# Kernel optimization log

Measured on AMD Instinct MI355X. Metric: run time of the kernel, lower is better.

Reference implementation:

```python
import jax, jax.numpy as jnp
import numpy as np

VOCAB, E, H, HOPS, HEADS = 32000, 128, 256, 3, 4
N, TM, WLEN, TQ = 32, 50, 20, 20


def _gru(x_tbe, h0, Wih, Whh, bih, bhh):
    # x_tbe: [T, B, E] time-major; h0: [B, H]. PyTorch GRU gate order (r, z, n).
    def step(h, xt):
        gi = xt @ Wih.T + bih
        gh = h @ Whh.T + bhh
        ir, iz, inn = jnp.split(gi, 3, axis=-1)
        hr, hz, hn = jnp.split(gh, 3, axis=-1)
        r = jax.nn.sigmoid(ir + hr)
        z = jax.nn.sigmoid(iz + hz)
        n = jnp.tanh(inn + r * hn)
        return (1.0 - z) * n + z * h, None
    h, _ = jax.lax.scan(step, h0, x_tbe)
    return h


def setup_inputs() -> dict:
    key = jax.random.key(0)
    ks = jax.random.split(key, 24)
    f32 = jnp.float32
    emb = jax.random.uniform(ks[0], (VOCAB, E), f32, -3 ** 0.5, 3 ** 0.5)
    emb = emb.at[0].set(0.0)  # padding_idx=0
    s = 0.05
    inp = {
        'stories': jax.random.randint(ks[1], (N, TM, WLEN), 0, VOCAB),
        'questions': jax.random.randint(ks[2], (N, TQ), 0, VOCAB),
        'emb': emb,
        'q_Wih': jax.random.normal(ks[3], (3 * H, E), f32) * s,
        'q_Whh': jax.random.normal(ks[4], (3 * H, H), f32) * s,
        'q_bih': jnp.zeros((3 * H,), f32),
        'q_bhh': jnp.zeros((3 * H,), f32),
        'i_Wih': jax.random.normal(ks[5], (3 * H, E), f32) * s,
        'i_Whh': jax.random.normal(ks[6], (3 * H, H), f32) * s,
        'i_bih': jnp.zeros((3 * H,), f32),
        'i_bhh': jnp.zeros((3 * H,), f32),
        'Wm': jax.random.normal(ks[7], (HOPS, HEADS, H, H), f32) * s,
        'Wo_w': jax.random.normal(ks[8], (HOPS, H, HEADS * H), f32) * s,
        'Wo_b': jnp.full((HOPS, H), 0.01, f32),
        'ft_W1': jax.random.normal(ks[9], (H, H), f32) * s,
        'ft_b1': jnp.full((H,), 0.01, f32),
        'ft_W2': jax.random.normal(ks[10], (H, H), f32) * s,
        'ft_b2': jnp.full((H,), 0.01, f32),
        'g_W1': jax.random.normal(ks[11], (3 * H, 3 * H), f32) * s,
        'g_b1': jnp.full((3 * H,), 0.01, f32),
        'g_W2': jax.random.normal(ks[12], (3 * H, 3 * H), f32) * s,
        'g_b2': jnp.full((3 * H,), 0.01, f32),
        'V_w': jax.random.normal(ks[13], (VOCAB, 3 * H), f32) * s,
    }
    return inp


def reference(stories, questions, emb, q_Wih, q_Whh, q_bih, q_bhh,
              i_Wih, i_Whh, i_bih, i_bhh, Wm, Wo_w, Wo_b,
              ft_W1, ft_b1, ft_W2, ft_b2, g_W1, g_b1, g_W2, g_b2, V_w):
    n, tm, _ = stories.shape
    h = i_Whh.shape[1]
    hops, heads = Wm.shape[0], Wm.shape[1]

    # ---- input module: per-batch-item GRU; hidden state carries across batch items (as in source loop) ----
    story_embs = emb[stories]  # [N, TM, W, E]
    def bstep(hid, se):  # se: [TM, W, E]
        hid2 = _gru(jnp.swapaxes(se, 0, 1), hid, i_Wih, i_Whh, i_bih, i_bhh)
        return hid2, hid2
    _, memory = jax.lax.scan(bstep, jnp.zeros((tm, h), emb.dtype), story_embs)  # [N, TM, H]

    # ---- question module ----
    q_emb = emb[questions]  # [N, TQ, E]
    q = _gru(jnp.swapaxes(q_emb, 0, 1), jnp.zeros((n, h), emb.dtype), q_Wih, q_Whh, q_bih, q_bhh)  # [N, H]

    def ft(x):
        return jax.nn.relu(jax.nn.relu(x @ ft_W1.T + ft_b1) @ ft_W2.T + ft_b2)

    # ---- multi-hop attention controllers ----
    o_k = ft(q)
    buffers = []
    for hp in range(hops):
        proj = jnp.tanh(jnp.einsum('ntd,hed->nhte', memory, Wm[hp]))      # [N,heads,TM,H]
        scores = jax.nn.softmax(jnp.einsum('nhte,ne->nht', proj, o_k), axis=-1)
        rep = jnp.einsum('nht,ntd->nhd', scores, memory)                   # [N,heads,H]
        buf = rep.reshape(n, heads * h) @ Wo_w[hp].T + Wo_b[hp]            # [N,H]
        buffers.append(buf)
        o_k = ft(buf)
    wb = jnp.stack(buffers, axis=1)  # [N, HOPS, H]

    # ---- RM: all-pairs relation MLP (dropout = identity in eval) ----
    npair = hops * hops
    left = jnp.broadcast_to(wb[:, None, :, :], (n, hops, hops, h)).reshape(n, npair, h)
    right = jnp.broadcast_to(wb[:, :, None, :], (n, hops, hops, h)).reshape(n, npair, h)
    qx = jnp.broadcast_to(q[:, None, :], (n, npair, h))
    comb = jnp.concatenate([left, right, qx], axis=-1)                     # [N, HOPS^2, 3H]
    g = jax.nn.relu(jax.nn.relu(comb @ g_W1.T + g_b1) @ g_W2.T + g_b2)
    reasoning = g.sum(axis=1)                                              # [N, 3H]
    return reasoning @ V_w.T                                               # [N, VOCAB]
```

## Files before the change

### kernel.cpp

```cpp
#include <hip/hip_runtime.h>
#include <cmath>

#define VOCABN 32000
#define EE 128
#define HH 256
#define H3 768
#define HOPSN 3
#define HEADSN 4
#define NB 32
#define TMN 50
#define WLENN 20
#define TQN 20
#define NPOS (NB*TMN*WLENN)
#define NQPOS (NB*TQN)

#define OFF_MEM    0
#define OFF_Q      (OFF_MEM + NB*TMN*HH)
#define OFF_OK     (OFF_Q + NB*HH)
#define OFF_WB     (OFF_OK + NB*HH)
#define OFF_REP    (OFF_WB + NB*HOPSN*HH)
#define OFF_REAS   (OFF_REP + NB*HEADSN*HH)
#define OFF_Y1     (OFF_REAS + NB*H3)
#define OFF_PROJ   (OFF_Y1 + NB*9*H3)
#define OFF_GI     (OFF_PROJ + NB*12*TMN*HH)

typedef __fp16 h2 __attribute__((ext_vector_type(2)));

__device__ __forceinline__ float sigm(float x) { return 1.f / (1.f + expf(-x)); }

__device__ __forceinline__ unsigned packh2(float x, float y) {
    h2 h = __builtin_amdgcn_cvt_pkrtz(x, y);
    return __builtin_bit_cast(unsigned, h);
}

__device__ __forceinline__ float fdot2u(unsigned a, unsigned b, float c) {
    return __builtin_amdgcn_fdot2(__builtin_bit_cast(h2, a),
                                  __builtin_bit_cast(h2, b), c, false);
}

#define LW(v, base, i8) { const float4 A_ = reinterpret_cast<const float4*>(base)[2*(i8)];     \
                          const float4 B_ = reinterpret_cast<const float4*>(base)[2*(i8)+1];   \
                          v.x = packh2(A_.x, A_.y); v.y = packh2(A_.z, A_.w);                  \
                          v.z = packh2(B_.x, B_.y); v.w = packh2(B_.z, B_.w); }

#define GIB 64
__global__ __launch_bounds__(768) void k_gi(const int* __restrict__ stories,
                                            const int* __restrict__ questions,
                                            const float* __restrict__ emb,
                                            const float* __restrict__ iWih,
                                            const float* __restrict__ qWih,
                                            const float* __restrict__ ibih, const float* __restrict__ ibhh,
                                            const float* __restrict__ qbih, const float* __restrict__ qbhh,
                                            float* __restrict__ ws)
{
    __shared__ unsigned xs[GIB][EE / 2];
    __fp16* __restrict__ gi = (__fp16*)(ws + OFF_GI);
    const int j = threadIdx.x;
    const bool isq = blockIdx.x >= (NPOS / GIB);
    const int pblk = isq ? (blockIdx.x - NPOS / GIB) : blockIdx.x;
    const int p0 = pblk * GIB;
    const size_t g0 = (isq ? (size_t)NPOS : 0) + (size_t)p0;
    const int* __restrict__ toks = isq ? (questions + p0) : (stories + p0);
    const float* __restrict__ Wih = isq ? qWih : iWih;
    const float* __restrict__ bih = isq ? qbih : ibih;
    const float* __restrict__ bhh = isq ? qbhh : ibhh;
    const float bias = (j < 2 * HH) ? (bih[j] + bhh[j]) : bih[j];
    const float* wrowp = Wih + (size_t)j * EE;
    uint4 v_0, v_1, v_2, v_3, v_4, v_5, v_6, v_7, v_8, v_9, v_10, v_11, v_12, v_13, v_14, v_15;
    LW(v_0, wrowp, 0)  LW(v_1, wrowp, 1)  LW(v_2, wrowp, 2)  LW(v_3, wrowp, 3)
    LW(v_4, wrowp, 4)  LW(v_5, wrowp, 5)  LW(v_6, wrowp, 6)  LW(v_7, wrowp, 7)
    LW(v_8, wrowp, 8)  LW(v_9, wrowp, 9)  LW(v_10, wrowp, 10) LW(v_11, wrowp, 11)
    LW(v_12, wrowp, 12) LW(v_13, wrowp, 13) LW(v_14, wrowp, 14) LW(v_15, wrowp, 15)

    for (int idx = j; idx < GIB * (EE / 2); idx += H3) {
        const int p = idx >> 6, c = idx & 63;
        const int tok = toks[p];
        const float2 e2 = reinterpret_cast<const float2*>(emb + (size_t)tok * EE)[c];
        xs[p][c] = packh2(e2.x, e2.y);
    }
    __syncthreads();

#define DOTG(i) { const uint4 xv = x4[i];                                     \
    acc = fdot2u(xv.x, v_##i.x, acc); acc = fdot2u(xv.y, v_##i.y, acc);       \
    acc = fdot2u(xv.z, v_##i.z, acc); acc = fdot2u(xv.w, v_##i.w, acc); }

    for (int p = 0; p < GIB; ++p) {
        const uint4* x4 = reinterpret_cast<const uint4*>(&xs[p][0]);
        float acc = bias;
        DOTG(0)  DOTG(1)  DOTG(2)  DOTG(3)  DOTG(4)  DOTG(5)  DOTG(6)  DOTG(7)
        DOTG(8)  DOTG(9)  DOTG(10) DOTG(11) DOTG(12) DOTG(13) DOTG(14) DOTG(15)
        gi[(g0 + p) * H3 + j] = (__fp16)acc;
    }
#undef DOTG
}

#define LDSF 22016
__global__ __attribute__((amdgpu_flat_work_group_size(512, 512), amdgpu_waves_per_eu(1, 1)))
void k_gru9(
    const float* __restrict__ iWhh, const float* __restrict__ qWhh,
    const float* __restrict__ ibhh, const float* __restrict__ qbhh,
    float* __restrict__ ws)
{
    __shared__ float ldsb[LDSF];
    unsigned* hp32 = (unsigned*)ldsb;
    float* red = ldsb + 128;
    const int tid = threadIdx.x;
    const int j = tid & 255, kh = tid >> 8;
    const int blk = blockIdx.x;
    const bool isq = blk >= TMN;
    const float* __restrict__ Whh = isq ? qWhh : iWhh;
    const float* row0 = Whh + (size_t)j * HH + kh * 128;
    const float* row1 = Whh + (size_t)(HH + j) * HH + kh * 128;
    const float* row2 = Whh + (size_t)(2 * HH + j) * HH + kh * 128;
    uint4 w0_0, w0_1, w0_2, w0_3, w0_4, w0_5, w0_6, w0_7,
          w0_8, w0_9, w0_10, w0_11, w0_12, w0_13, w0_14, w0_15;
    uint4 w1_0, w1_1, w1_2, w1_3, w1_4, w1_5, w1_6, w1_7,
          w1_8, w1_9, w1_10, w1_11, w1_12, w1_13, w1_14, w1_15;
    uint4 w2_0, w2_1, w2_2, w2_3, w2_4, w2_5, w2_6, w2_7,
          w2_8, w2_9, w2_10, w2_11, w2_12, w2_13, w2_14, w2_15;
    LW(w0_0, row0, 0)  LW(w0_1, row0, 1)  LW(w0_2, row0, 2)  LW(w0_3, row0, 3)
    LW(w0_4, row0, 4)  LW(w0_5, row0, 5)  LW(w0_6, row0, 6)  LW(w0_7, row0, 7)
    LW(w0_8, row0, 8)  LW(w0_9, row0, 9)  LW(w0_10, row0, 10) LW(w0_11, row0, 11)
    LW(w0_12, row0, 12) LW(w0_13, row0, 13) LW(w0_14, row0, 14) LW(w0_15, row0, 15)
    LW(w1_0, row1, 0)  LW(w1_1, row1, 1)  LW(w1_2, row1, 2)  LW(w1_3, row1, 3)
    LW(w1_4, row1, 4)  LW(w1_5, row1, 5)  LW(w1_6, row1, 6)  LW(w1_7, row1, 7)
    LW(w1_8, row1, 8)  LW(w1_9, row1, 9)  LW(w1_10, row1, 10) LW(w1_11, row1, 11)
    LW(w1_12, row1, 12) LW(w1_13, row1, 13) LW(w1_14, row1, 14) LW(w1_15, row1, 15)
    LW(w2_0, row2, 0)  LW(w2_1, row2, 1)  LW(w2_2, row2, 2)  LW(w2_3, row2, 3)
    LW(w2_4, row2, 4)  LW(w2_5, row2, 5)  LW(w2_6, row2, 6)  LW(w2_7, row2, 7)
    LW(w2_8, row2, 8)  LW(w2_9, row2, 9)  LW(w2_10, row2, 10) LW(w2_11, row2, 11)
    LW(w2_12, row2, 12) LW(w2_13, row2, 13) LW(w2_14, row2, 14) LW(w2_15, row2, 15)

    float bnH = 0.f, hstate = 0.f;
    if (kh == 0) bnH = (isq ? qbhh : ibhh)[2 * HH + j];
    if (tid < HH / 2) hp32[tid] = 0u;
    const __fp16* __restrict__ gib = (const __fp16*)(ws + OFF_GI)
                                     + (isq ? (size_t)NPOS * H3 : 0);
    float* __restrict__ memv = ws + OFF_MEM;
    float* __restrict__ qv   = ws + OFF_Q;
    __syncthreads();

#define DOT(i) { const uint4 hv = hp4[kh * 16 + (i)];                        \
    a0 = fdot2u(hv.x, w0_##i.x, a0); a0 = fdot2u(hv.y, w0_##i.y, a0);        \
    a0 = fdot2u(hv.z, w0_##i.z, a0); a0 = fdot2u(hv.w, w0_##i.w, a0);        \
    a1 = fdot2u(hv.x, w1_##i.x, a1); a1 = fdot2u(hv.y, w1_##i.y, a1);        \
    a1 = fdot2u(hv.z, w1_##i.z, a1); a1 = fdot2u(hv.w, w1_##i.w, a1);        \
    a2 = fdot2u(hv.x, w2_##i.x, a2); a2 = fdot2u(hv.y, w2_##i.y, a2);        \
    a2 = fdot2u(hv.z, w2_##i.z, a2); a2 = fdot2u(hv.w, w2_##i.w, a2); }

    const int nOuter = isq ? 1 : NB;
    const int c = isq ? (blk - TMN) : blk;
    for (int n = 0; n < nOuter; ++n) {
        for (int t = 0; t < WLENN; ++t) {
            const int pos = isq ? (c * TQN + t) : ((n * TMN + c) * WLENN + t);
            float gir = 0.f, giz = 0.f, gin = 0.f;
            if (kh == 0) {
                const size_t gb = (size_t)pos * H3;
                gir = (float)gib[gb + j];
                giz = (float)gib[gb + HH + j];
                gin = (float)gib[gb + 2 * HH + j];
            }
            float a0 = 0.f, a1 = 0.f, a2 = 0.f;
            const uint4* hp4 = reinterpret_cast<const uint4*>(hp32);
            DOT(0)  DOT(1)  DOT(2)  DOT(3)  DOT(4)  DOT(5)  DOT(6)  DOT(7)
            DOT(8)  DOT(9)  DOT(10) DOT(11) DOT(12) DOT(13) DOT(14) DOT(15)
            if (kh == 1) { red[j * 5 + 0] = a0; red[j * 5 + 1] = a1; red[j * 5 + 2] = a2; }
            __syncthreads();
            if (kh == 0) {
                const float* rr = red + j * 5;
                const float r  = sigm(a0 + rr[0] + gir);
                const float z  = sigm(a1 + rr[1] + giz);
                const float nn = tanhf(gin + r * (a2 + rr[2] + bnH));
                hstate = (1.f - z) * nn + z * hstate;
                reinterpret_cast<__fp16*>(hp32)[j] = (__fp16)hstate;
                if (t == WLENN - 1) {
                    if (isq) qv[c * HH + j] = hstate;
                    else     memv[(size_t)(n * TMN + c) * HH + j] = hstate;
                }
            }
            __syncthreads();
        }
    }
#undef DOT
}

__global__ __launch_bounds__(256) void k_ft(const float* __restrict__ src, float* __restrict__ dst,
                                            const float* __restrict__ W1, const float* __restrict__ b1,
                                            const float* __restrict__ W2, const float* __restrict__ b2)
{
    __shared__ float xr[HH];
    __shared__ float y1[HH];
    const int n = blockIdx.x, j = threadIdx.x;
    xr[j] = src[n * HH + j];
    __syncthreads();
    float acc = b1[j];
    const float4* w1 = reinterpret_cast<const float4*>(W1 + j * HH);
    #pragma unroll 4
    for (int k4 = 0; k4 < HH / 4; ++k4) {
        const float4 w = w1[k4];
        const float4 x = *reinterpret_cast<const float4*>(&xr[k4 * 4]);
        acc = fmaf(x.x, w.x, fmaf(x.y, w.y, fmaf(x.z, w.z, fmaf(x.w, w.w, acc))));
    }
    y1[j] = fmaxf(acc, 0.f);
    __syncthreads();
    acc = b2[j];
    const float4* w2 = reinterpret_cast<const float4*>(W2 + j * HH);
    #pragma unroll 4
    for (int k4 = 0; k4 < HH / 4; ++k4) {
        const float4 w = w2[k4];
        const float4 x = *reinterpret_cast<const float4*>(&y1[k4 * 4]);
        acc = fmaf(x.x, w.x, fmaf(x.y, w.y, fmaf(x.z, w.z, fmaf(x.w, w.w, acc))));
    }
    dst[n * HH + j] = fmaxf(acc, 0.f);
}

__global__ __launch_bounds__(256) void k_proj(const float* __restrict__ Wm, float* __restrict__ ws)
{
    __shared__ float mem_s[TMN][HH];
    const int n = blockIdx.x / 12, he = blockIdx.x % 12;
    const int e = threadIdx.x;
    const float* __restrict__ memory = ws + OFF_MEM + n * TMN * HH;
    for (int idx = e; idx < TMN * HH; idx += HH)
        (&mem_s[0][0])[idx] = memory[idx];
    __syncthreads();
    float p[TMN];
    #pragma unroll
    for (int t = 0; t < TMN; ++t) p[t] = 0.f;
    const float4* wrow = reinterpret_cast<const float4*>(Wm + ((size_t)he * HH + e) * HH);
    for (int d4 = 0; d4 < HH / 4; ++d4) {
        const float4 w = wrow[d4];
        #pragma unroll
        for (int t = 0; t < TMN; ++t) {
            const float4 m = *reinterpret_cast<const float4*>(&mem_s[t][d4 * 4]);
            p[t] = fmaf(m.x, w.x, fmaf(m.y, w.y, fmaf(m.z, w.z, fmaf(m.w, w.w, p[t]))));
        }
    }
    float* __restrict__ proj = ws + OFF_PROJ + ((size_t)(n * 12 + he) * TMN) * HH;
    #pragma unroll
    for (int t = 0; t < TMN; ++t) proj[t * HH + e] = tanhf(p[t]);
}

__global__ __launch_bounds__(256) void k_attn2(float* __restrict__ ws, int hp)
{
    __shared__ float wred[4][TMN];
    __shared__ float sc[TMN];
    const int n = blockIdx.x / HEADSN, hh = blockIdx.x % HEADSN;
    const int e = threadIdx.x;
    const float* __restrict__ proj = ws + OFF_PROJ + ((size_t)(n * 12 + hp * HEADSN + hh) * TMN) * HH;
    const float* __restrict__ memory = ws + OFF_MEM + n * TMN * HH;
    const float okv = (ws + OFF_OK)[n * HH + e];
    const int lane = e & 63, wv = e >> 6;
    #pragma unroll 10
    for (int t = 0; t < TMN; ++t) {
        float v = proj[t * HH + e] * okv;
        #pragma unroll
        for (int off = 32; off > 0; off >>= 1) v += __shfl_xor(v, off);
        if (lane == 0) wred[wv][t] = v;
    }
    __syncthreads();
    if (e < TMN) sc[e] = wred[0][e] + wred[1][e] + wred[2][e] + wred[3][e];
    __syncthreads();
    if (e == 0) {
        float mx = sc[0];
        for (int t = 1; t < TMN; ++t) mx = fmaxf(mx, sc[t]);
        float sum = 0.f;
        for (int t = 0; t < TMN; ++t) { const float ex = expf(sc[t] - mx); sc[t] = ex; sum += ex; }
        const float inv = 1.f / sum;
        for (int t = 0; t < TMN; ++t) sc[t] *= inv;
    }
    __syncthreads();
    float r = 0.f;
    #pragma unroll 10
    for (int t = 0; t < TMN; ++t) r = fmaf(sc[t], memory[t * HH + e], r);
    (ws + OFF_REP)[(n * HEADSN + hh) * HH + e] = r;
}

__global__ __launch_bounds__(256) void k_buf(const float* __restrict__ Wo_w, const float* __restrict__ Wo_b,
                                             const float* __restrict__ W1, const float* __restrict__ b1,
                                             const float* __restrict__ W2, const float* __restrict__ b2,
                                             float* __restrict__ ws, int hp)
{
    __shared__ float repf[HEADSN * HH];
    __shared__ float bufs[HH];
    __shared__ float y1[HH];
    const int n = blockIdx.x, j = threadIdx.x;
    const float* __restrict__ rep = ws + OFF_REP + n * HEADSN * HH;
    for (int idx = j; idx < HEADSN * HH; idx += HH) repf[idx] = rep[idx];
    __syncthreads();
    float acc = Wo_b[hp * HH + j];
    const float4* wrow = reinterpret_cast<const float4*>(Wo_w + ((size_t)hp * HH + j) * (HEADSN * HH));
    #pragma unroll 4
    for (int c4 = 0; c4 < HEADSN * HH / 4; ++c4) {
        const float4 w = wrow[c4];
        const float4 x = *reinterpret_cast<const float4*>(&repf[c4 * 4]);
        acc = fmaf(x.x, w.x, fmaf(x.y, w.y, fmaf(x.z, w.z, fmaf(x.w, w.w, acc))));
    }
    (ws + OFF_WB)[(n * HOPSN + hp) * HH + j] = acc;
    bufs[j] = acc;
    __syncthreads();
    float a1 = b1[j];
    const float4* w1 = reinterpret_cast<const float4*>(W1 + j * HH);
    #pragma unroll 4
    for (int k4 = 0; k4 < HH / 4; ++k4) {
        const float4 w = w1[k4];
        const float4 x = *reinterpret_cast<const float4*>(&bufs[k4 * 4]);
        a1 = fmaf(x.x, w.x, fmaf(x.y, w.y, fmaf(x.z, w.z, fmaf(x.w, w.w, a1))));
    }
    y1[j] = fmaxf(a1, 0.f);
    __syncthreads();
    float a2 = b2[j];
    const float4* w2 = reinterpret_cast<const float4*>(W2 + j * HH);
    #pragma unroll 4
    for (int k4 = 0; k4 < HH / 4; ++k4) {
        const float4 w = w2[k4];
        const float4 x = *reinterpret_cast<const float4*>(&y1[k4 * 4]);
        a2 = fmaf(x.x, w.x, fmaf(x.y, w.y, fmaf(x.z, w.z, fmaf(x.w, w.w, a2))));
    }
    (ws + OFF_OK)[n * HH + j] = fmaxf(a2, 0.f);
}

__global__ __launch_bounds__(256) void k_rm1(const float* __restrict__ gW1, const float* __restrict__ gb1,
                                             float* __restrict__ ws)
{
    __shared__ float comb[9 * H3];
    const int n = blockIdx.x / 3, ot = blockIdx.x % 3;
    const int o = ot * 256 + threadIdx.x;
    const float* __restrict__ wb = ws + OFF_WB + n * HOPSN * HH;
    const float* __restrict__ qv = ws + OFF_Q + n * HH;
    for (int idx = threadIdx.x; idx < 9 * H3; idx += 256) {
        const int p = idx / H3, cc = idx - p * H3;
        const int ii = p / 3, jj = p % 3;
        float v;
        if (cc < HH)           v = wb[jj * HH + cc];
        else if (cc < 2 * HH)  v = wb[ii * HH + (cc - HH)];
        else                   v = qv[cc - 2 * HH];
        comb[idx] = v;
    }
    __syncthreads();
    float acc[9];
    const float b = gb1[o];
    #pragma unroll
    for (int p = 0; p < 9; ++p) acc[p] = b;
    const float4* w1 = reinterpret_cast<const float4*>(gW1 + (size_t)o * H3);
    for (int c4 = 0; c4 < H3 / 4; ++c4) {
        const float4 w = w1[c4];
        #pragma unroll
        for (int p = 0; p < 9; ++p) {
            const float4 x = *reinterpret_cast<const float4*>(&comb[p * H3 + c4 * 4]);
            acc[p] = fmaf(x.x, w.x, fmaf(x.y, w.y, fmaf(x.z, w.z, fmaf(x.w, w.w, acc[p]))));
        }
    }
    float* __restrict__ y1 = ws + OFF_Y1 + (size_t)n * 9 * H3;
    #pragma unroll
    for (int p = 0; p < 9; ++p) y1[p * H3 + o] = fmaxf(acc[p], 0.f);
}

__global__ __launch_bounds__(256) void k_rm2(const float* __restrict__ gW2, const float* __restrict__ gb2,
                                             float* __restrict__ ws)
{
    __shared__ float y1s[9 * H3];
    const int n = blockIdx.x / 3, ot = blockIdx.x % 3;
    const int o = ot * 256 + threadIdx.x;
    const float* __restrict__ y1 = ws + OFF_Y1 + (size_t)n * 9 * H3;
    for (int idx = threadIdx.x; idx < 9 * H3; idx += 256) y1s[idx] = y1[idx];
    __syncthreads();
    float acc[9];
    const float b = gb2[o];
    #pragma unroll
    for (int p = 0; p < 9; ++p) acc[p] = b;
    const float4* w2 = reinterpret_cast<const float4*>(gW2 + (size_t)o * H3);
    for (int c4 = 0; c4 < H3 / 4; ++c4) {
        const float4 w = w2[c4];
        #pragma unroll
        for (int p = 0; p < 9; ++p) {
            const float4 x = *reinterpret_cast<const float4*>(&y1s[p * H3 + c4 * 4]);
            acc[p] = fmaf(x.x, w.x, fmaf(x.y, w.y, fmaf(x.z, w.z, fmaf(x.w, w.w, acc[p]))));
        }
    }
    float s = 0.f;
    #pragma unroll
    for (int p = 0; p < 9; ++p) s += fmaxf(acc[p], 0.f);
    (ws + OFF_REAS)[n * H3 + o] = s;
}

#define RST 36
__global__ __launch_bounds__(256) void k_out(const float* __restrict__ V_w, const float* __restrict__ ws,
                                             float* __restrict__ out)
{
    __shared__ float rsT[H3 * RST];
    const int tid = threadIdx.x;
    const int v = blockIdx.x * 128 + (tid & 127);
    const int nh = tid >> 7;
    for (int idx = tid; idx < NB * H3; idx += 256) {
        const int n = idx / H3, d = idx - n * H3;
        rsT[d * RST + n] = (ws + OFF_REAS)[idx];
    }
    __syncthreads();
    float acc[16];
    #pragma unroll
    for (int i = 0; i < 16; ++i) acc[i] = 0.f;
    const float4* vw = reinterpret_cast<const float4*>(V_w + (size_t)v * H3);
    for (int d4 = 0; d4 < H3 / 4; ++d4) {
        const float4 w = vw[d4];
        #pragma unroll
        for (int dd = 0; dd < 4; ++dd) {
            const float wd = (dd == 0) ? w.x : (dd == 1) ? w.y : (dd == 2) ? w.z : w.w;
            const float* rr = &rsT[(d4 * 4 + dd) * RST + nh * 16];
            #pragma unroll
            for (int q = 0; q < 4; ++q) {
                const float4 r4 = *reinterpret_cast<const float4*>(rr + 4 * q);
                acc[4 * q + 0] = fmaf(wd, r4.x, acc[4 * q + 0]);
                acc[4 * q + 1] = fmaf(wd, r4.y, acc[4 * q + 1]);
                acc[4 * q + 2] = fmaf(wd, r4.z, acc[4 * q + 2]);
                acc[4 * q + 3] = fmaf(wd, r4.w, acc[4 * q + 3]);
            }
        }
    }
    #pragma unroll
    for (int i = 0; i < 16; ++i)
        out[(size_t)(nh * 16 + i) * VOCABN + v] = acc[i];
}

extern "C" void kernel_launch(void* const* d_in, const int* in_sizes, int n_in,
                              void* d_out, int out_size, void* d_ws, size_t ws_size,
                              hipStream_t stream)
{
    const int*   stories   = (const int*)d_in[0];
    const int*   questions = (const int*)d_in[1];
    const float* emb   = (const float*)d_in[2];
    const float* qWih  = (const float*)d_in[3];
    const float* qWhh  = (const float*)d_in[4];
    const float* qbih  = (const float*)d_in[5];
    const float* qbhh  = (const float*)d_in[6];
    const float* iWih  = (const float*)d_in[7];
    const float* iWhh  = (const float*)d_in[8];
    const float* ibih  = (const float*)d_in[9];
    const float* ibhh  = (const float*)d_in[10];
    const float* Wm    = (const float*)d_in[11];
    const float* Wo_w  = (const float*)d_in[12];
    const float* Wo_b  = (const float*)d_in[13];
    const float* ftW1  = (const float*)d_in[14];
    const float* ftb1  = (const float*)d_in[15];
    const float* ftW2  = (const float*)d_in[16];
    const float* ftb2  = (const float*)d_in[17];
    const float* gW1   = (const float*)d_in[18];
    const float* gb1   = (const float*)d_in[19];
    const float* gW2   = (const float*)d_in[20];
    const float* gb2   = (const float*)d_in[21];
    const float* V_w   = (const float*)d_in[22];
    float* ws  = (float*)d_ws;
    float* out = (float*)d_out;

    hipLaunchKernelGGL(k_gi, dim3((NPOS + NQPOS) / GIB), dim3(H3), 0, stream,
                       stories, questions, emb, iWih, qWih, ibih, ibhh, qbih, qbhh, ws);
    hipLaunchKernelGGL(k_gru9, dim3(TMN + NB), dim3(512), 0, stream,
                       iWhh, qWhh, ibhh, qbhh, ws);
    hipLaunchKernelGGL(k_ft, dim3(NB), dim3(HH), 0, stream, ws + OFF_Q, ws + OFF_OK, ftW1, ftb1, ftW2, ftb2);
    hipLaunchKernelGGL(k_proj, dim3(NB * 12), dim3(256), 0, stream, Wm, ws);
    for (int hp = 0; hp < HOPSN; ++hp) {
        hipLaunchKernelGGL(k_attn2, dim3(NB * HEADSN), dim3(256), 0, stream, ws, hp);
        hipLaunchKernelGGL(k_buf, dim3(NB), dim3(256), 0, stream, Wo_w, Wo_b, ftW1, ftb1, ftW2, ftb2, ws, hp);
    }
    hipLaunchKernelGGL(k_rm1, dim3(NB * 3), dim3(256), 0, stream, gW1, gb1, ws);
    hipLaunchKernelGGL(k_rm2, dim3(NB * 3), dim3(256), 0, stream, gW2, gb2, ws);
    hipLaunchKernelGGL(k_out, dim3(VOCABN / 128), dim3(256), 0, stream, V_w, ws, out);
}
```

Measured before the change: 1.363 ms.

## Stream prepacked fp16 GRU recurrent weights from global memory each step

Adds a prepack kernel that converts both Whh matrices to fp16 in a coalesced, interleaved layout in the workspace. The GRU kernel no longer holds 48 uint4 of weights in registers. It reloads them from global memory (L2-resident) at every timestep, using a software-pipelined load/dot schedule and an asm barrier to stop the loads being hoisted. The aim is to relieve register pressure, at the cost of repeated global/L2 traffic in the latency-bound sequential loop. It also adds one extra launch.

```diff
diff --git a/kernel.cpp b/kernel.cpp
--- a/kernel.cpp
+++ b/kernel.cpp
@@ -23,6 +23,8 @@
 #define OFF_Y1     (OFF_REAS + NB*H3)
 #define OFF_PROJ   (OFF_Y1 + NB*9*H3)
 #define OFF_GI     (OFF_PROJ + NB*12*TMN*HH)
+#define OFF_WPK    (OFF_GI + (NPOS+NQPOS)*H3/2)
+#define NWPK4      24576
 
 typedef __fp16 h2 __attribute__((ext_vector_type(2)));
 
@@ -42,6 +44,31 @@
                           const float4 B_ = reinterpret_cast<const float4*>(base)[2*(i8)+1];   \
                           v.x = packh2(A_.x, A_.y); v.y = packh2(A_.z, A_.w);                  \
                           v.z = packh2(B_.x, B_.y); v.w = packh2(B_.z, B_.w); }
+
+__global__ __launch_bounds__(256) void k_prepack(const float* __restrict__ iWhh,
+                                                 const float* __restrict__ qWhh,
+                                                 float* __restrict__ ws)
+{
+    uint4* __restrict__ wpk = (uint4*)(ws + OFF_WPK);
+    const int idx = blockIdx.x * 256 + threadIdx.x;
+    const bool isq = idx >= NWPK4;
+    const int r = isq ? idx - NWPK4 : idx;
+    const float* __restrict__ W = isq ? qWhh : iWhh;
+    const int j  = r & 255;
+    const int q  = r >> 8;
+    const int c  = q % 6;
+    const int s  = (q / 6) & 7;
+    const int kh = q / 48;
+    const int g  = c >> 1;
+    const int pb = s * 8 + (c & 1) * 4;
+    const float* row = W + ((size_t)(g * HH + j)) * HH + kh * 128;
+    uint4 o;
+    o.x = packh2(row[(pb + 0) * 2], row[(pb + 0) * 2 + 1]);
+    o.y = packh2(row[(pb + 1) * 2], row[(pb + 1) * 2 + 1]);
+    o.z = packh2(row[(pb + 2) * 2], row[(pb + 2) * 2 + 1]);
+    o.w = packh2(row[(pb + 3) * 2], row[(pb + 3) * 2 + 1]);
+    wpk[idx] = o;
+}
 
 #define GIB 64
 __global__ __launch_bounds__(768) void k_gi(const int* __restrict__ stories,
@@ -94,42 +121,17 @@
 #undef DOTG
 }
 
-#define LDSF 22016
-__global__ __attribute__((amdgpu_flat_work_group_size(512, 512), amdgpu_waves_per_eu(1, 1)))
-void k_gru9(
-    const float* __restrict__ iWhh, const float* __restrict__ qWhh,
+__global__ __launch_bounds__(512) void k_gru11(
     const float* __restrict__ ibhh, const float* __restrict__ qbhh,
     float* __restrict__ ws)
 {
-    __shared__ float ldsb[LDSF];
-    unsigned* hp32 = (unsigned*)ldsb;
-    float* red = ldsb + 128;
+    __shared__ unsigned hp32[HH / 2];
+    __shared__ float red[HH * 5];
     const int tid = threadIdx.x;
     const int j = tid & 255, kh = tid >> 8;
     const int blk = blockIdx.x;
     const bool isq = blk >= TMN;
-    const float* __restrict__ Whh = isq ? qWhh : iWhh;
-    const float* row0 = Whh + (size_t)j * HH + kh * 128;
-    const float* row1 = Whh + (size_t)(HH + j) * HH + kh * 128;
-    const float* row2 = Whh + (size_t)(2 * HH + j) * HH + kh * 128;
-    uint4 w0_0, w0_1, w0_2, w0_3, w0_4, w0_5, w0_6, w0_7,
-          w0_8, w0_9, w0_10, w0_11, w0_12, w0_13, w0_14, w0_15;
-    uint4 w1_0, w1_1, w1_2, w1_3, w1_4, w1_5, w1_6, w1_7,
-          w1_8, w1_9, w1_10, w1_11, w1_12, w1_13, w1_14, w1_15;
-    uint4 w2_0, w2_1, w2_2, w2_3, w2_4, w2_5, w2_6, w2_7,
-          w2_8, w2_9, w2_10, w2_11, w2_12, w2_13, w2_14, w2_15;
-    LW(w0_0, row0, 0)  LW(w0_1, row0, 1)  LW(w0_2, row0, 2)  LW(w0_3, row0, 3)
-    LW(w0_4, row0, 4)  LW(w0_5, row0, 5)  LW(w0_6, row0, 6)  LW(w0_7, row0, 7)
-    LW(w0_8, row0, 8)  LW(w0_9, row0, 9)  LW(w0_10, row0, 10) LW(w0_11, row0, 11)
-    LW(w0_12, row0, 12) LW(w0_13, row0, 13) LW(w0_14, row0, 14) LW(w0_15, row0, 15)
-    LW(w1_0, row1, 0)  LW(w1_1, row1, 1)  LW(w1_2, row1, 2)  LW(w1_3, row1, 3)
-    LW(w1_4, row1, 4)  LW(w1_5, row1, 5)  LW(w1_6, row1, 6)  LW(w1_7, row1, 7)
-    LW(w1_8, row1, 8)  LW(w1_9, row1, 9)  LW(w1_10, row1, 10) LW(w1_11, row1, 11)
-    LW(w1_12, row1, 12) LW(w1_13, row1, 13) LW(w1_14, row1, 14) LW(w1_15, row1, 15)
-    LW(w2_0, row2, 0)  LW(w2_1, row2, 1)  LW(w2_2, row2, 2)  LW(w2_3, row2, 3)
-    LW(w2_4, row2, 4)  LW(w2_5, row2, 5)  LW(w2_6, row2, 6)  LW(w2_7, row2, 7)
-    LW(w2_8, row2, 8)  LW(w2_9, row2, 9)  LW(w2_10, row2, 10) LW(w2_11, row2, 11)
-    LW(w2_12, row2, 12) LW(w2_13, row2, 13) LW(w2_14, row2, 14) LW(w2_15, row2, 15)
+    const uint4* __restrict__ wpk0 = (const uint4*)(ws + OFF_WPK) + (isq ? NWPK4 : 0);
 
     float bnH = 0.f, hstate = 0.f;
     if (kh == 0) bnH = (isq ? qbhh : ibhh)[2 * HH + j];
@@ -140,13 +142,23 @@
     float* __restrict__ qv   = ws + OFF_Q;
     __syncthreads();
 
-#define DOT(i) { const uint4 hv = hp4[kh * 16 + (i)];                        \
-    a0 = fdot2u(hv.x, w0_##i.x, a0); a0 = fdot2u(hv.y, w0_##i.y, a0);        \
-    a0 = fdot2u(hv.z, w0_##i.z, a0); a0 = fdot2u(hv.w, w0_##i.w, a0);        \
-    a1 = fdot2u(hv.x, w1_##i.x, a1); a1 = fdot2u(hv.y, w1_##i.y, a1);        \
-    a1 = fdot2u(hv.z, w1_##i.z, a1); a1 = fdot2u(hv.w, w1_##i.w, a1);        \
-    a2 = fdot2u(hv.x, w2_##i.x, a2); a2 = fdot2u(hv.y, w2_##i.y, a2);        \
-    a2 = fdot2u(hv.z, w2_##i.z, a2); a2 = fdot2u(hv.w, w2_##i.w, a2); }
+#define WIX(s, c) ((((kh) * 8 + (s)) * 6 + (c)) * 256 + j)
+#define LD(P, s) const uint4 P##_0 = wp[WIX(s,0)], P##_1 = wp[WIX(s,1)], P##_2 = wp[WIX(s,2)], \
+                             P##_3 = wp[WIX(s,3)], P##_4 = wp[WIX(s,4)], P##_5 = wp[WIX(s,5)];
+#define DOTS(P, s) { const uint4 h0 = hp4[kh * 16 + 2 * (s)];                    \
+                     const uint4 h1 = hp4[kh * 16 + 2 * (s) + 1];                \
+    g0 = fdot2u(h0.x, P##_0.x, g0); g0 = fdot2u(h0.y, P##_0.y, g0);              \
+    g0 = fdot2u(h0.z, P##_0.z, g0); g0 = fdot2u(h0.w, P##_0.w, g0);              \
+    g0 = fdot2u(h1.x, P##_1.x, g0); g0 = fdot2u(h1.y, P##_1.y, g0);              \
+    g0 = fdot2u(h1.z, P##_1.z, g0); g0 = fdot2u(h1.w, P##_1.w, g0);              \
+    g1 = fdot2u(h0.x, P##_2.x, g1); g1 = fdot2u(h0.y, P##_2.y, g1);              \
+    g1 = fdot2u(h0.z, P##_2.z, g1); g1 = fdot2u(h0.w, P##_2.w, g1);              \
+    g1 = fdot2u(h1.x, P##_3.x, g1); g1 = fdot2u(h1.y, P##_3.y, g1);              \
+    g1 = fdot2u(h1.z, P##_3.z, g1); g1 = fdot2u(h1.w, P##_3.w, g1);              \
+    g2 = fdot2u(h0.x, P##_4.x, g2); g2 = fdot2u(h0.y, P##_4.y, g2);              \
+    g2 = fdot2u(h0.z, P##_4.z, g2); g2 = fdot2u(h0.w, P##_4.w, g2);              \
+    g2 = fdot2u(h1.x, P##_5.x, g2); g2 = fdot2u(h1.y, P##_5.y, g2);              \
+    g2 = fdot2u(h1.z, P##_5.z, g2); g2 = fdot2u(h1.w, P##_5.w, g2); }
 
     const int nOuter = isq ? 1 : NB;
     const int c = isq ? (blk - TMN) : blk;
@@ -160,17 +172,27 @@
                 giz = (float)gib[gb + HH + j];
                 gin = (float)gib[gb + 2 * HH + j];
             }
-            float a0 = 0.f, a1 = 0.f, a2 = 0.f;
+            size_t wpa = (size_t)wpk0;
+            asm volatile("" : "+v"(wpa));
+            const uint4* __restrict__ wp = (const uint4*)wpa;
             const uint4* hp4 = reinterpret_cast<const uint4*>(hp32);
-            DOT(0)  DOT(1)  DOT(2)  DOT(3)  DOT(4)  DOT(5)  DOT(6)  DOT(7)
-            DOT(8)  DOT(9)  DOT(10) DOT(11) DOT(12) DOT(13) DOT(14) DOT(15)
-            if (kh == 1) { red[j * 5 + 0] = a0; red[j * 5 + 1] = a1; red[j * 5 + 2] = a2; }
+            float g0 = 0.f, g1 = 0.f, g2 = 0.f;
+            LD(wA, 0) LD(wB, 1) LD(wC, 2)
+            LD(wD, 3) DOTS(wA, 0)
+            LD(wE, 4) DOTS(wB, 1)
+            LD(wF, 5) DOTS(wC, 2)
+            LD(wG, 6) DOTS(wD, 3)
+            LD(wH, 7) DOTS(wE, 4)
+            DOTS(wF, 5)
+            DOTS(wG, 6)
+            DOTS(wH, 7)
+            if (kh == 1) { red[j * 5 + 0] = g0; red[j * 5 + 1] = g1; red[j * 5 + 2] = g2; }
             __syncthreads();
             if (kh == 0) {
                 const float* rr = red + j * 5;
-                const float r  = sigm(a0 + rr[0] + gir);
-                const float z  = sigm(a1 + rr[1] + giz);
-                const float nn = tanhf(gin + r * (a2 + rr[2] + bnH));
+                const float r  = sigm(g0 + rr[0] + gir);
+                const float z  = sigm(g1 + rr[1] + giz);
+                const float nn = tanhf(gin + r * (g2 + rr[2] + bnH));
                 hstate = (1.f - z) * nn + z * hstate;
                 reinterpret_cast<__fp16*>(hp32)[j] = (__fp16)hstate;
                 if (t == WLENN - 1) {
@@ -181,7 +203,9 @@
             __syncthreads();
         }
     }
-#undef DOT
+#undef DOTS
+#undef LD
+#undef WIX
 }
 
 __global__ __launch_bounds__(256) void k_ft(const float* __restrict__ src, float* __restrict__ dst,
@@ -451,10 +475,10 @@
     float* ws  = (float*)d_ws;
     float* out = (float*)d_out;
 
+    hipLaunchKernelGGL(k_prepack, dim3(2 * NWPK4 / 256), dim3(256), 0, stream, iWhh, qWhh, ws);
     hipLaunchKernelGGL(k_gi, dim3((NPOS + NQPOS) / GIB), dim3(H3), 0, stream,
                        stories, questions, emb, iWih, qWih, ibih, ibhh, qbih, qbhh, ws);
-    hipLaunchKernelGGL(k_gru9, dim3(TMN + NB), dim3(512), 0, stream,
-                       iWhh, qWhh, ibhh, qbhh, ws);
+    hipLaunchKernelGGL(k_gru11, dim3(TMN + NB), dim3(512), 0, stream, ibhh, qbhh, ws);
     hipLaunchKernelGGL(k_ft, dim3(NB), dim3(HH), 0, stream, ws + OFF_Q, ws + OFF_OK, ftW1, ftb1, ftW2, ftb2);
     hipLaunchKernelGGL(k_proj, dim3(NB * 12), dim3(256), 0, stream, Wm, ws);
     for (int hp = 0; hp < HOPSN; ++hp) {
```

After: 2.868 ms. 110% more time.

## Restructure GRU recurrence to one thread per gate row with LDS weight spill

Applied to the files above, without the earlier changes.

The recurrent GRU kernel now uses 768 threads per block, one per Whh output row over the full 256-wide hidden dimension, instead of 512 threads splitting K in halves across three gates. Twenty uint4 weight chunks per row stay in registers and the remaining twelve go to LDS, with four independent accumulators to shorten dependency chains. The cross-thread partial-sum reduction is replaced by writing gate pre-activations to LDS, and the first 256 threads then apply the nonlinearities. This aims to remove the K-split reduction and add parallelism per step, at the cost of extra LDS reads on every timestep and higher register pressure.

```diff
diff --git a/kernel.cpp b/kernel.cpp
--- a/kernel.cpp
+++ b/kernel.cpp
@@ -94,94 +94,96 @@
 #undef DOTG
 }
 
-#define LDSF 22016
-__global__ __attribute__((amdgpu_flat_work_group_size(512, 512), amdgpu_waves_per_eu(1, 1)))
-void k_gru9(
+#define NWR 20
+#define NWS 12
+#define LDSD (NWS*768*4 + 128 + 768 + 256)
+__global__ __launch_bounds__(768) void k_gru12(
     const float* __restrict__ iWhh, const float* __restrict__ qWhh,
     const float* __restrict__ ibhh, const float* __restrict__ qbhh,
     float* __restrict__ ws)
 {
-    __shared__ float ldsb[LDSF];
-    unsigned* hp32 = (unsigned*)ldsb;
-    float* red = ldsb + 128;
+    __shared__ float ldsb[LDSD];
+    uint4* __restrict__ wlds = (uint4*)ldsb;
+    unsigned* __restrict__ hp32 = (unsigned*)(ldsb + NWS * 768 * 4);
+    float* __restrict__ gv    = ldsb + NWS * 768 * 4 + 128;
+    float* __restrict__ gin_s = ldsb + NWS * 768 * 4 + 128 + 768;
     const int tid = threadIdx.x;
-    const int j = tid & 255, kh = tid >> 8;
+    const int j = tid & 255, g = tid >> 8;
     const int blk = blockIdx.x;
     const bool isq = blk >= TMN;
     const float* __restrict__ Whh = isq ? qWhh : iWhh;
-    const float* row0 = Whh + (size_t)j * HH + kh * 128;
-    const float* row1 = Whh + (size_t)(HH + j) * HH + kh * 128;
-    const float* row2 = Whh + (size_t)(2 * HH + j) * HH + kh * 128;
-    uint4 w0_0, w0_1, w0_2, w0_3, w0_4, w0_5, w0_6, w0_7,
-          w0_8, w0_9, w0_10, w0_11, w0_12, w0_13, w0_14, w0_15;
-    uint4 w1_0, w1_1, w1_2, w1_3, w1_4, w1_5, w1_6, w1_7,
-          w1_8, w1_9, w1_10, w1_11, w1_12, w1_13, w1_14, w1_15;
-    uint4 w2_0, w2_1, w2_2, w2_3, w2_4, w2_5, w2_6, w2_7,
-          w2_8, w2_9, w2_10, w2_11, w2_12, w2_13, w2_14, w2_15;
-    LW(w0_0, row0, 0)  LW(w0_1, row0, 1)  LW(w0_2, row0, 2)  LW(w0_3, row0, 3)
-    LW(w0_4, row0, 4)  LW(w0_5, row0, 5)  LW(w0_6, row0, 6)  LW(w0_7, row0, 7)
-    LW(w0_8, row0, 8)  LW(w0_9, row0, 9)  LW(w0_10, row0, 10) LW(w0_11, row0, 11)
-    LW(w0_12, row0, 12) LW(w0_13, row0, 13) LW(w0_14, row0, 14) LW(w0_15, row0, 15)
-    LW(w1_0, row1, 0)  LW(w1_1, row1, 1)  LW(w1_2, row1, 2)  LW(w1_3, row1, 3)
-    LW(w1_4, row1, 4)  LW(w1_5, row1, 5)  LW(w1_6, row1, 6)  LW(w1_7, row1, 7)
-    LW(w1_8, row1, 8)  LW(w1_9, row1, 9)  LW(w1_10, row1, 10) LW(w1_11, row1, 11)
-    LW(w1_12, row1, 12) LW(w1_13, row1, 13) LW(w1_14, row1, 14) LW(w1_15, row1, 15)
-    LW(w2_0, row2, 0)  LW(w2_1, row2, 1)  LW(w2_2, row2, 2)  LW(w2_3, row2, 3)
-    LW(w2_4, row2, 4)  LW(w2_5, row2, 5)  LW(w2_6, row2, 6)  LW(w2_7, row2, 7)
-    LW(w2_8, row2, 8)  LW(w2_9, row2, 9)  LW(w2_10, row2, 10) LW(w2_11, row2, 11)
-    LW(w2_12, row2, 12) LW(w2_13, row2, 13) LW(w2_14, row2, 14) LW(w2_15, row2, 15)
-
+    const float* rowp = Whh + (size_t)tid * HH;
+
+    uint4 w_0, w_1, w_2, w_3, w_4, w_5, w_6, w_7, w_8, w_9,
+          w_10, w_11, w_12, w_13, w_14, w_15, w_16, w_17, w_18, w_19;
+    LW(w_0, rowp, 0)   LW(w_1, rowp, 1)   LW(w_2, rowp, 2)   LW(w_3, rowp, 3)
+    LW(w_4, rowp, 4)   LW(w_5, rowp, 5)   LW(w_6, rowp, 6)   LW(w_7, rowp, 7)
+    LW(w_8, rowp, 8)   LW(w_9, rowp, 9)   LW(w_10, rowp, 10) LW(w_11, rowp, 11)
+    LW(w_12, rowp, 12) LW(w_13, rowp, 13) LW(w_14, rowp, 14) LW(w_15, rowp, 15)
+    LW(w_16, rowp, 16) LW(w_17, rowp, 17) LW(w_18, rowp, 18) LW(w_19, rowp, 19)
+    #pragma unroll
+    for (int s = 0; s < NWS; ++s) {
+        uint4 tmp;
+        LW(tmp, rowp, NWR + s)
+        wlds[s * 768 + tid] = tmp;
+    }
     float bnH = 0.f, hstate = 0.f;
-    if (kh == 0) bnH = (isq ? qbhh : ibhh)[2 * HH + j];
+    if (g == 2) bnH = (isq ? qbhh : ibhh)[2 * HH + j];
     if (tid < HH / 2) hp32[tid] = 0u;
     const __fp16* __restrict__ gib = (const __fp16*)(ws + OFF_GI)
                                      + (isq ? (size_t)NPOS * H3 : 0);
     float* __restrict__ memv = ws + OFF_MEM;
     float* __restrict__ qv   = ws + OFF_Q;
-    __syncthreads();
-
-#define DOT(i) { const uint4 hv = hp4[kh * 16 + (i)];                        \
-    a0 = fdot2u(hv.x, w0_##i.x, a0); a0 = fdot2u(hv.y, w0_##i.y, a0);        \
-    a0 = fdot2u(hv.z, w0_##i.z, a0); a0 = fdot2u(hv.w, w0_##i.w, a0);        \
-    a1 = fdot2u(hv.x, w1_##i.x, a1); a1 = fdot2u(hv.y, w1_##i.y, a1);        \
-    a1 = fdot2u(hv.z, w1_##i.z, a1); a1 = fdot2u(hv.w, w1_##i.w, a1);        \
-    a2 = fdot2u(hv.x, w2_##i.x, a2); a2 = fdot2u(hv.y, w2_##i.y, a2);        \
-    a2 = fdot2u(hv.z, w2_##i.z, a2); a2 = fdot2u(hv.w, w2_##i.w, a2); }
+    const uint4* __restrict__ myw = wlds + tid;
+    __syncthreads();
+
+#define DR(i, ac) { const uint4 hv = hp4[i];                                 \
+    ac = fdot2u(hv.x, w_##i.x, ac); ac = fdot2u(hv.y, w_##i.y, ac);          \
+    ac = fdot2u(hv.z, w_##i.z, ac); ac = fdot2u(hv.w, w_##i.w, ac); }
 
     const int nOuter = isq ? 1 : NB;
     const int c = isq ? (blk - TMN) : blk;
     for (int n = 0; n < nOuter; ++n) {
         for (int t = 0; t < WLENN; ++t) {
             const int pos = isq ? (c * TQN + t) : ((n * TMN + c) * WLENN + t);
-            float gir = 0.f, giz = 0.f, gin = 0.f;
-            if (kh == 0) {
-                const size_t gb = (size_t)pos * H3;
-                gir = (float)gib[gb + j];
-                giz = (float)gib[gb + HH + j];
-                gin = (float)gib[gb + 2 * HH + j];
+            const float giv = (float)gib[(size_t)pos * H3 + tid];
+            const uint4* hp4 = reinterpret_cast<const uint4*>(hp32);
+            float a0 = 0.f, a1 = 0.f, a2 = 0.f, a3 = 0.f;
+            DR(0, a0)  DR(1, a1)  DR(2, a2)  DR(3, a3)
+            DR(4, a0)  DR(5, a1)  DR(6, a2)  DR(7, a3)
+            DR(8, a0)  DR(9, a1)  DR(10, a2) DR(11, a3)
+            DR(12, a0) DR(13, a1) DR(14, a2) DR(15, a3)
+            DR(16, a0) DR(17, a1) DR(18, a2) DR(19, a3)
+            #pragma unroll
+            for (int s = 0; s < NWS; ++s) {
+                const uint4 wv = myw[s * 768];
+                const uint4 hv = hp4[NWR + s];
+                a0 = fdot2u(hv.x, wv.x, a0); a1 = fdot2u(hv.y, wv.y, a1);
+                a2 = fdot2u(hv.z, wv.z, a2); a3 = fdot2u(hv.w, wv.w, a3);
             }
-            float a0 = 0.f, a1 = 0.f, a2 = 0.f;
-            const uint4* hp4 = reinterpret_cast<const uint4*>(hp32);
-            DOT(0)  DOT(1)  DOT(2)  DOT(3)  DOT(4)  DOT(5)  DOT(6)  DOT(7)
-            DOT(8)  DOT(9)  DOT(10) DOT(11) DOT(12) DOT(13) DOT(14) DOT(15)
-            if (kh == 1) { red[j * 5 + 0] = a0; red[j * 5 + 1] = a1; red[j * 5 + 2] = a2; }
+            const float acc = (a0 + a1) + (a2 + a3);
+            if (g == 2) {
+                gv[tid] = acc + bnH;
+                gin_s[j] = giv;
+            } else {
+                gv[tid] = acc + giv;
+            }
             __syncthreads();
-            if (kh == 0) {
-                const float* rr = red + j * 5;
-                const float r  = sigm(a0 + rr[0] + gir);
-                const float z  = sigm(a1 + rr[1] + giz);
-                const float nn = tanhf(gin + r * (a2 + rr[2] + bnH));
+            if (tid < HH) {
+                const float r  = sigm(gv[tid]);
+                const float z  = sigm(gv[HH + tid]);
+                const float nn = tanhf(gin_s[tid] + r * gv[2 * HH + tid]);
                 hstate = (1.f - z) * nn + z * hstate;
-                reinterpret_cast<__fp16*>(hp32)[j] = (__fp16)hstate;
+                reinterpret_cast<__fp16*>(hp32)[tid] = (__fp16)hstate;
                 if (t == WLENN - 1) {
-                    if (isq) qv[c * HH + j] = hstate;
-                    else     memv[(size_t)(n * TMN + c) * HH + j] = hstate;
+                    if (isq) qv[c * HH + tid] = hstate;
+                    else     memv[(size_t)(n * TMN + c) * HH + tid] = hstate;
                 }
             }
             __syncthreads();
         }
     }
-#undef DOT
+#undef DR
 }
 
 __global__ __launch_bounds__(256) void k_ft(const float* __restrict__ src, float* __restrict__ dst,
@@ -453,7 +455,7 @@
 
     hipLaunchKernelGGL(k_gi, dim3((NPOS + NQPOS) / GIB), dim3(H3), 0, stream,
                        stories, questions, emb, iWih, qWih, ibih, ibhh, qbih, qbhh, ws);
-    hipLaunchKernelGGL(k_gru9, dim3(TMN + NB), dim3(512), 0, stream,
+    hipLaunchKernelGGL(k_gru12, dim3(TMN + NB), dim3(H3), 0, stream,
                        iWhh, qWhh, ibhh, qbhh, ws);
     hipLaunchKernelGGL(k_ft, dim3(NB), dim3(HH), 0, stream, ws + OFF_Q, ws + OFF_OK, ftW1, ftb1, ftW2, ftb2);
     hipLaunchKernelGGL(k_proj, dim3(NB * 12), dim3(256), 0, stream, Wm, ws);
```

Measured after the change: 1.543 ms. 1.13x slower.
